# Kernel optimization log

Hardware: AMD Instinct MI355X
Metric: run time of the kernel (lower is better)

Reference implementation:

```python
import jax, jax.numpy as jnp
import numpy as np

ALPHA = 0.25        # focal alpha
GAMMA = 2.0         # focal gamma
POS_T = 0.5         # max_iou positive threshold
NEG_T = 0.4         # max_iou negative threshold
SL1_BETA = 1.0 / 9.0  # smooth_l1 with sigma=3
EPS = 1e-6

N, T, A, C = 8, 64, 65536, 80


def setup_inputs() -> dict:
    key = jax.random.key(0)
    ks = jax.random.split(key, 6)
    labels = jax.random.randint(ks[0], (N, T), 1, C)
    y_true = jax.nn.one_hot(labels, C, dtype=jnp.float32)
    xy = jax.random.uniform(ks[1], (N, T, 2)) * 0.7
    wh = jax.random.uniform(ks[2], (N, T, 2)) * 0.25 + 0.02
    bbox_true = jnp.concatenate([xy, xy + wh], axis=-1)
    valid = (jnp.arange(T) < 24).astype(jnp.float32)  # zero-pad remaining GT rows
    bbox_true = bbox_true * valid[None, :, None]
    axy = jax.random.uniform(ks[3], (A, 2)) * 0.9
    awh = jax.random.uniform(jax.random.fold_in(ks[3], 1), (A, 2)) * 0.15 + 0.02
    anchors = jnp.concatenate([axy, axy + awh], axis=-1)
    y_pred = jax.random.normal(ks[4], (N, A, C), dtype=jnp.float32)
    bbox_pred = jax.random.normal(ks[5], (N, A, 4), dtype=jnp.float32) * 0.1
    return {"y_true": y_true, "bbox_true": bbox_true, "y_pred": y_pred,
            "bbox_pred": bbox_pred, "anchors": anchors}


def _iou(b1, b2):
    # b1: (T,4), b2: (A,4) -> (T,A)
    a1 = jnp.maximum(b1[:, 2] - b1[:, 0], 0) * jnp.maximum(b1[:, 3] - b1[:, 1], 0)
    a2 = jnp.maximum(b2[:, 2] - b2[:, 0], 0) * jnp.maximum(b2[:, 3] - b2[:, 1], 0)
    lt = jnp.maximum(b1[:, None, :2], b2[None, :, :2])
    rb = jnp.minimum(b1[:, None, 2:], b2[None, :, 2:])
    wh = jnp.maximum(rb - lt, 0.0)
    inter = wh[..., 0] * wh[..., 1]
    union = a1[:, None] + a2[None, :] - inter
    return inter / jnp.maximum(union, 1e-10)


def _bbox2delta(boxes, anchors):
    # standard (dx, dy, dw, dh) encoding, mean=0 / std=1
    wa = jnp.maximum(anchors[:, 2] - anchors[:, 0], EPS)
    ha = jnp.maximum(anchors[:, 3] - anchors[:, 1], EPS)
    cxa = anchors[:, 0] + 0.5 * wa
    cya = anchors[:, 1] + 0.5 * ha
    wt = jnp.maximum(boxes[:, 2] - boxes[:, 0], EPS)
    ht = jnp.maximum(boxes[:, 3] - boxes[:, 1], EPS)
    cxt = boxes[:, 0] + 0.5 * (boxes[:, 2] - boxes[:, 0])
    cyt = boxes[:, 1] + 0.5 * (boxes[:, 3] - boxes[:, 1])
    return jnp.stack([(cxt - cxa) / wa, (cyt - cya) / ha,
                      jnp.log(wt / wa), jnp.log(ht / ha)], axis=-1)


def _encode_target(y_true_i, bbox_true_i, anchors):
    # y_true_i: (T,C), bbox_true_i: (T,4), anchors: (A,4)
    valid = jnp.any(bbox_true_i > 0, axis=-1)                 # (T,)
    iou = jnp.where(valid[:, None], _iou(bbox_true_i, anchors), -1.0)  # (T,A)
    max_iou = iou.max(axis=0)                                  # (A,)
    assigned = iou.argmax(axis=0)                              # (A,) gt index per anchor
    pos = max_iou >= POS_T
    neg = (max_iou < NEG_T)
    # low-quality matching: each valid gt's best anchor is positive for that gt
    gt_best = iou.argmax(axis=1)                               # (T,)
    gt_best_iou = iou.max(axis=1)
    lq = valid & (gt_best_iou > 0)
    assigned = assigned.at[gt_best].set(jnp.where(lq, jnp.arange(bbox_true_i.shape[0]), assigned[gt_best]))
    pos = pos.at[gt_best].set(jnp.where(lq, True, pos[gt_best]))
    neg = neg & (~pos)
    state = jnp.where(pos, 1, jnp.where(neg, -1, 0)).astype(jnp.int8)[:, None]  # (A,1)
    # class target: background one-hot [1,0,...,0], positives get gt label
    bg = jnp.zeros((anchors.shape[0], y_true_i.shape[-1]), jnp.float32).at[:, 0].set(1.0)
    yt = jnp.where(pos[:, None], y_true_i[assigned], bg)       # (A,C)
    delta = _bbox2delta(bbox_true_i[assigned], anchors)        # (A,4)
    bt = jnp.where(pos[:, None], delta, 0.0)
    return state, yt, bt


def _focal_bce(y_true, logits):
    # elementwise sigmoid focal loss
    ce = jnp.maximum(logits, 0) - logits * y_true + jnp.log1p(jnp.exp(-jnp.abs(logits)))
    p = jax.nn.sigmoid(logits)
    p_t = y_true * p + (1.0 - y_true) * (1.0 - p)
    a_t = y_true * ALPHA + (1.0 - y_true) * (1.0 - ALPHA)
    return a_t * jnp.power(1.0 - p_t, GAMMA) * ce


def _smooth_l1(y_true, y_pred):
    d = jnp.abs(y_true - y_pred)
    return jnp.where(d < SL1_BETA, 0.5 * d * d / SL1_BETA, d - 0.5 * SL1_BETA)


def _sanitize(x):
    return jnp.where(jnp.isnan(x) | jnp.isinf(x), 0.0, x)


def reference(y_true, bbox_true, y_pred, bbox_pred, anchors):
    state, yt, bt = jax.vmap(lambda a, b: _encode_target(a, b, anchors))(y_true, bbox_true)
    positive_w = (state == 1).astype(y_pred.dtype)   # (N,A,1)
    target_w = (state != 0).astype(y_pred.dtype)     # (N,A,1)
    avg_factor = jnp.sum(jnp.maximum(jnp.sum(positive_w, axis=-2), 1.0))
    yt = yt * positive_w                              # background=False zeroes non-positives
    cls = jnp.sum(_focal_bce(yt, y_pred) * target_w) / avg_factor
    box = jnp.sum(_smooth_l1(bt, bbox_pred) * positive_w) / avg_factor
    return _sanitize(cls), _sanitize(box)
```

## Files before the change

### kernel.cpp

```cpp
#include <hip/hip_runtime.h>
#include <hip/hip_bf16.h>
#include <math.h>

#define NB 8
#define TB 64
#define AB 65536
#define CB 80
#define EPSF 1e-6f

#define WS_POSCNT_OFF 4096
#define WS_LABEL_OFF  4608
#define WS_CODE_OFF   8192
#define WS_PCLS_OFF   (WS_CODE_OFF + NB*AB*4)
#define WS_PCCLS_OFF  (WS_PCLS_OFF + 4096*4)
#define WS_PCBOX_OFF  (WS_PCCLS_OFF + 2048*4)
#define WS_MEMSET_BYTES 4608

__device__ __forceinline__ float focal0(float l) {
    float q  = __expf(-fabsf(l));
    float r  = __builtin_amdgcn_rcpf(1.f + q);
    float lg = __logf(r);
    float ce = fmaxf(l, 0.f) - lg;
    float p  = (l >= 0.f) ? r : 1.f - r;
    return 0.75f * p * p * ce;
}
__device__ __forceinline__ float focal_diff(float l) {
    float q  = __expf(-fabsf(l));
    float r  = __builtin_amdgcn_rcpf(1.f + q);
    float lg = __logf(r);
    float m  = fmaxf(l, 0.f);
    float p  = (l >= 0.f) ? r : 1.f - r;
    float f0 = 0.75f * p * p * (m - lg);
    float om = 1.f - p;
    float f1 = 0.25f * om * om * (m - l - lg);
    return f1 - f0;
}
__device__ __forceinline__ float smooth_l1(float x) {
    float d = fabsf(x);
    return d < (1.f / 9.f) ? 4.5f * d * d : d - (0.5f / 9.f);
}

__global__ __launch_bounds__(256) void assign_kernel(
    const float* __restrict__ bbox_true,
    const float* __restrict__ anchors,
    int*   __restrict__ code,
    unsigned long long* __restrict__ gt_key)
{
    __shared__ float4 s_box[TB];
    __shared__ float  s_a1[TB];
    __shared__ unsigned long long s_key[TB];

    const int blk   = blockIdx.x;
    const int i     = blk >> 8;
    const int abase = (blk & 255) << 8;
    const int tid   = threadIdx.x;

    if (tid < TB) {
        float4 b = ((const float4*)bbox_true)[i * TB + tid];
        s_box[tid] = b;
        s_a1[tid]  = fmaxf(b.z - b.x, 0.f) * fmaxf(b.w - b.y, 0.f);
        s_key[tid] = 0ull;
    }
    __syncthreads();

    const int a = abase + tid;
    const float4 an = ((const float4*)anchors)[a];
    const float a2 = fmaxf(an.z - an.x, 0.f) * fmaxf(an.w - an.y, 0.f);

    float best = -1.0f;
    int bestt = 0;
    #pragma unroll 8
    for (int t = 0; t < TB; ++t) {
        float4 b = s_box[t];
        float lx = fmaxf(b.x, an.x), ly = fmaxf(b.y, an.y);
        float rx = fminf(b.z, an.z), ry = fminf(b.w, an.w);
        float w = fmaxf(rx - lx, 0.f), h = fmaxf(ry - ly, 0.f);
        float inter = w * h;
        float uni = s_a1[t] + a2 - inter;
        float iou = inter * __builtin_amdgcn_rcpf(fmaxf(uni, 1e-10f));
        if (iou > 0.f) {
            unsigned long long key =
                ((unsigned long long)__float_as_uint(iou) << 32) |
                (unsigned long long)((unsigned)a ^ 0xFFFFFFFFu);
            if (key > s_key[t])
                atomicMax(&s_key[t], key);
        }
        if (iou > best) { best = iou; bestt = t; }
    }
    bool pos = best >= 0.5f;
    bool neg = best < 0.4f;
    code[i * AB + a] = pos ? bestt : (neg ? -1 : -2);

    __syncthreads();
    if (tid < TB) {
        unsigned long long k = s_key[tid];
        if (k) atomicMax(&gt_key[i * TB + tid], k);
    }
}

__global__ void lq_label_kernel(const unsigned long long* __restrict__ gt_key,
                                const float* __restrict__ y_true,
                                int* __restrict__ code,
                                int* __restrict__ labels)
{
    __shared__ unsigned long long sk[NB * TB];
    const int tid = threadIdx.x;
    sk[tid] = gt_key[tid];

    const float* row = y_true + (size_t)tid * CB;
    int lab = 0;
    for (int c = 0; c < CB; ++c)
        if (row[c] > 0.5f) lab = c;
    labels[tid] = lab;

    __syncthreads();
    const int i = tid >> 6, t = tid & 63;
    unsigned long long k = sk[tid];
    if (k) {
        unsigned a = (unsigned)(k & 0xFFFFFFFFull) ^ 0xFFFFFFFFu;
        bool win = true;
        for (int t2 = t + 1; t2 < TB; ++t2) {
            unsigned long long k2 = sk[(i << 6) | t2];
            if (k2 && (((unsigned)(k2 & 0xFFFFFFFFull) ^ 0xFFFFFFFFu) == a))
                win = false;
        }
        if (win) code[i * AB + (int)a] = t;
    }
}

__global__ __launch_bounds__(256) void stream_kernel(
    const float4* __restrict__ yp4,
    float* __restrict__ p_cls)
{
    const int tid = threadIdx.x;
    const int g0  = blockIdx.x * 256 + tid;
    float acc = 0.f;
    #pragma unroll
    for (int j = 0; j < 10; ++j) {
        float4 v = yp4[g0 + j * 1048576];
        acc += focal0(v.x) + focal0(v.y) + focal0(v.z) + focal0(v.w);
    }
    for (int off = 32; off > 0; off >>= 1) acc += __shfl_down(acc, off);
    __shared__ float s[4];
    int wave = tid >> 6, lane = tid & 63;
    if (lane == 0) s[wave] = acc;
    __syncthreads();
    if (tid == 0) p_cls[blockIdx.x] = s[0] + s[1] + s[2] + s[3];
}

__global__ __launch_bounds__(256) void corr_kernel(
    const float* __restrict__ y_pred,
    const float* __restrict__ bbox_true,
    const float* __restrict__ bbox_pred,
    const float* __restrict__ anchors,
    const int*   __restrict__ code,
    const int*   __restrict__ labels,
    float* __restrict__ p_ccls,
    float* __restrict__ p_cbox,
    int*   __restrict__ pos_cnt)
{
    const int tid = threadIdx.x;
    const int b   = blockIdx.x;
    const int i   = b >> 8;
    const int g   = b * 256 + tid;
    const int a   = g & (AB - 1);

    const int cv = code[g];
    float cls_c = 0.f, box_c = 0.f;
    int posc = 0;

    if (cv >= 0) {
        posc = 1;
        int c = labels[i * TB + cv];
        float l = y_pred[(size_t)g * CB + c];
        cls_c = focal_diff(l);

        float4 bt = ((const float4*)bbox_true)[i * TB + cv];
        float4 an = ((const float4*)anchors)[a];
        float wa = fmaxf(an.z - an.x, EPSF), ha = fmaxf(an.w - an.y, EPSF);
        float cxa = an.x + 0.5f * wa,  cya = an.y + 0.5f * ha;
        float wt = fmaxf(bt.z - bt.x, EPSF), ht = fmaxf(bt.w - bt.y, EPSF);
        float cxt = bt.x + 0.5f * (bt.z - bt.x), cyt = bt.y + 0.5f * (bt.w - bt.y);
        float d0 = (cxt - cxa) / wa, d1 = (cyt - cya) / ha;
        float d2 = __logf(wt / wa),  d3 = __logf(ht / ha);
        float4 bp = ((const float4*)bbox_pred)[g];
        box_c = smooth_l1(d0 - bp.x) + smooth_l1(d1 - bp.y) +
                smooth_l1(d2 - bp.z) + smooth_l1(d3 - bp.w);
    } else if (cv == -2) {
        const float4* yp4 = (const float4*)(y_pred + (size_t)g * CB);
        float s = 0.f;
        #pragma unroll 4
        for (int k = 0; k < 20; ++k) {
            float4 v = yp4[k];
            s += focal0(v.x) + focal0(v.y) + focal0(v.z) + focal0(v.w);
        }
        cls_c = -s;
    }

    for (int off = 32; off > 0; off >>= 1) {
        cls_c += __shfl_down(cls_c, off);
        box_c += __shfl_down(box_c, off);
        posc  += __shfl_down(posc, off);
    }
    __shared__ float sc[4], sb[4];
    __shared__ int   sp[4];
    int wave = tid >> 6, lane = tid & 63;
    if (lane == 0) { sc[wave] = cls_c; sb[wave] = box_c; sp[wave] = posc; }
    __syncthreads();
    if (tid == 0) {
        p_ccls[b] = sc[0] + sc[1] + sc[2] + sc[3];
        p_cbox[b] = sb[0] + sb[1] + sb[2] + sb[3];
        int p = sp[0] + sp[1] + sp[2] + sp[3];
        if (p) atomicAdd(&pos_cnt[i], p);
    }
}

__global__ __launch_bounds__(256) void reduce_kernel(
    const float* __restrict__ p_cls,
    const float* __restrict__ p_ccls,
    const float* __restrict__ p_cbox,
    const int*   __restrict__ pos_cnt,
    float* __restrict__ out)
{
    const int tid = threadIdx.x;
    const int wave = tid >> 6, lane = tid & 63;

    double c = 0.0, bx = 0.0;
    #pragma unroll
    for (int j = 0; j < 16; ++j) c += (double)p_cls[tid + j * 256];
    #pragma unroll
    for (int j = 0; j < 8; ++j)  c += (double)p_ccls[tid + j * 256];
    #pragma unroll
    for (int j = 0; j < 8; ++j)  bx += (double)p_cbox[tid + j * 256];

    for (int off = 32; off > 0; off >>= 1) {
        c  += __shfl_down(c, off);
        bx += __shfl_down(bx, off);
    }
    __shared__ double sc[4], sb[4];
    if (lane == 0) { sc[wave] = c; sb[wave] = bx; }
    __syncthreads();
    if (tid == 0) {
        float avg = 0.f;
        for (int i = 0; i < NB; ++i) avg += fmaxf((float)pos_cnt[i], 1.0f);
        double ct = sc[0] + sc[1] + sc[2] + sc[3];
        double bt = sb[0] + sb[1] + sb[2] + sb[3];
        float cf = (float)(ct / (double)avg);
        float bf = (float)(bt / (double)avg);
        if (isnan(cf) || isinf(cf)) cf = 0.f;
        if (isnan(bf) || isinf(bf)) bf = 0.f;
        out[0] = cf;
        out[1] = bf;
    }
}

extern "C" void kernel_launch(void* const* d_in, const int* in_sizes, int n_in,
                              void* d_out, int out_size, void* d_ws, size_t ws_size,
                              hipStream_t stream) {
    const float* y_true    = (const float*)d_in[0];
    const float* bbox_true = (const float*)d_in[1];
    const float* y_pred    = (const float*)d_in[2];
    const float* bbox_pred = (const float*)d_in[3];
    const float* anchors   = (const float*)d_in[4];
    float* out = (float*)d_out;

    char* ws = (char*)d_ws;
    unsigned long long* gt_key = (unsigned long long*)ws;
    int*   pos_cnt = (int*)(ws + WS_POSCNT_OFF);
    int*   labels  = (int*)(ws + WS_LABEL_OFF);
    int*   code    = (int*)(ws + WS_CODE_OFF);
    float* p_cls   = (float*)(ws + WS_PCLS_OFF);
    float* p_ccls  = (float*)(ws + WS_PCCLS_OFF);
    float* p_cbox  = (float*)(ws + WS_PCBOX_OFF);

    hipMemsetAsync(ws, 0, WS_MEMSET_BYTES, stream);

    assign_kernel<<<NB * AB / 256, 256, 0, stream>>>(bbox_true, anchors, code, gt_key);
    lq_label_kernel<<<1, NB * TB, 0, stream>>>(gt_key, y_true, code, labels);
    stream_kernel<<<4096, 256, 0, stream>>>((const float4*)y_pred, p_cls);
    corr_kernel<<<NB * AB / 256, 256, 0, stream>>>(
        y_pred, bbox_true, bbox_pred, anchors, code, labels,
        p_ccls, p_cbox, pos_cnt);
    reduce_kernel<<<1, 256, 0, stream>>>(p_cls, p_ccls, p_cbox, pos_cnt, out);
}
```

Before: 334.1 us.

## Compact positive/ignore anchors into lists and drop the dense correction pass

```diff
diff --git a/kernel.cpp b/kernel.cpp
--- a/kernel.cpp
+++ b/kernel.cpp
@@ -8,31 +8,28 @@
 #define CB 80
 #define EPSF 1e-6f
 
-#define WS_POSCNT_OFF 4096
+#define WS_CNT_OFF    4096
 #define WS_LABEL_OFF  4608
 #define WS_CODE_OFF   8192
-#define WS_PCLS_OFF   (WS_CODE_OFF + NB*AB*4)
-#define WS_PCCLS_OFF  (WS_PCLS_OFF + 4096*4)
-#define WS_PCBOX_OFF  (WS_PCCLS_OFF + 2048*4)
+#define WS_PLIST_OFF  (WS_CODE_OFF + NB*AB*4)
+#define WS_ILIST_OFF  (WS_PLIST_OFF + 525312*4)
+#define WS_PCLS_OFF   (WS_ILIST_OFF + 525312*4)
 #define WS_MEMSET_BYTES 4608
 
 __device__ __forceinline__ float focal0(float l) {
-    float q  = __expf(-fabsf(l));
-    float r  = __builtin_amdgcn_rcpf(1.f + q);
-    float lg = __logf(r);
-    float ce = fmaxf(l, 0.f) - lg;
-    float p  = (l >= 0.f) ? r : 1.f - r;
-    return 0.75f * p * p * ce;
+    float u  = __expf(l);
+    float r  = __builtin_amdgcn_rcpf(1.f + u);
+    float p  = 1.f - r;
+    float lg = __log2f(r);
+    return p * p * lg * -0.5198603854f;
 }
 __device__ __forceinline__ float focal_diff(float l) {
-    float q  = __expf(-fabsf(l));
-    float r  = __builtin_amdgcn_rcpf(1.f + q);
-    float lg = __logf(r);
-    float m  = fmaxf(l, 0.f);
-    float p  = (l >= 0.f) ? r : 1.f - r;
-    float f0 = 0.75f * p * p * (m - lg);
-    float om = 1.f - p;
-    float f1 = 0.25f * om * om * (m - l - lg);
+    float u  = __expf(l);
+    float r  = __builtin_amdgcn_rcpf(1.f + u);
+    float p  = 1.f - r;
+    float sp = -0.6931471806f * __log2f(r);
+    float f1 = 0.25f * r * r * (sp - l);
+    float f0 = 0.75f * p * p * sp;
     return f1 - f0;
 }
 __device__ __forceinline__ float smooth_l1(float x) {
@@ -44,7 +41,10 @@
     const float* __restrict__ bbox_true,
     const float* __restrict__ anchors,
     int*   __restrict__ code,
-    unsigned long long* __restrict__ gt_key)
+    unsigned long long* __restrict__ gt_key,
+    int*   __restrict__ cnts,
+    int*   __restrict__ pos_list,
+    int*   __restrict__ ign_list)
 {
     __shared__ float4 s_box[TB];
     __shared__ float  s_a1[TB];
@@ -87,9 +87,17 @@
         }
         if (iou > best) { best = iou; bestt = t; }
     }
+    const int g = i * AB + a;
     bool pos = best >= 0.5f;
     bool neg = best < 0.4f;
-    code[i * AB + a] = pos ? bestt : (neg ? -1 : -2);
+    code[g] = pos ? bestt : (neg ? -1 : -2);
+    if (pos) {
+        int idx = atomicAdd(&cnts[0], 1);
+        pos_list[idx] = g;
+    } else if (!neg) {
+        int idx = atomicAdd(&cnts[1], 1);
+        ign_list[idx] = g;
+    }
 
     __syncthreads();
     if (tid < TB) {
@@ -101,7 +109,9 @@
 __global__ void lq_label_kernel(const unsigned long long* __restrict__ gt_key,
                                 const float* __restrict__ y_true,
                                 int* __restrict__ code,
-                                int* __restrict__ labels)
+                                int* __restrict__ labels,
+                                int* __restrict__ cnts,
+                                int* __restrict__ pos_list)
 {
     __shared__ unsigned long long sk[NB * TB];
     const int tid = threadIdx.x;
@@ -124,12 +134,22 @@
             if (k2 && (((unsigned)(k2 & 0xFFFFFFFFull) ^ 0xFFFFFFFFu) == a))
                 win = false;
         }
-        if (win) code[i * AB + (int)a] = t;
+        if (win) {
+            int g = i * AB + (int)a;
+            int pre = code[g];
+            code[g] = t;
+            if (pre < 0) {
+                int idx = atomicAdd(&cnts[0], 1);
+                pos_list[idx] = g | ((pre == -2) ? (1 << 30) : 0);
+            }
+        }
     }
 }
 
 __global__ __launch_bounds__(256) void stream_kernel(
     const float4* __restrict__ yp4,
+    const int*    __restrict__ ign_list,
+    const int*    __restrict__ cnts,
     float* __restrict__ p_cls)
 {
     const int tid = threadIdx.x;
@@ -140,6 +160,13 @@
         float4 v = yp4[g0 + j * 1048576];
         acc += focal0(v.x) + focal0(v.y) + focal0(v.z) + focal0(v.w);
     }
+    const int work = cnts[1] * 20;
+    for (int w = g0; w < work; w += 4096 * 256) {
+        int e = w / 20, ch = w - e * 20;
+        int g = ign_list[e];
+        float4 v = yp4[g * 20 + ch];
+        acc -= focal0(v.x) + focal0(v.y) + focal0(v.z) + focal0(v.w);
+    }
     for (int off = 32; off > 0; off >>= 1) acc += __shfl_down(acc, off);
     __shared__ float s[4];
     int wave = tid >> 6, lane = tid & 63;
@@ -148,34 +175,48 @@
     if (tid == 0) p_cls[blockIdx.x] = s[0] + s[1] + s[2] + s[3];
 }
 
-__global__ __launch_bounds__(256) void corr_kernel(
+__global__ __launch_bounds__(256) void reduce_kernel(
+    const float* __restrict__ p_cls,
+    const int*   __restrict__ cnts,
+    const int*   __restrict__ pos_list,
+    const int*   __restrict__ code,
+    const int*   __restrict__ labels,
     const float* __restrict__ y_pred,
     const float* __restrict__ bbox_true,
     const float* __restrict__ bbox_pred,
     const float* __restrict__ anchors,
-    const int*   __restrict__ code,
-    const int*   __restrict__ labels,
-    float* __restrict__ p_ccls,
-    float* __restrict__ p_cbox,
-    int*   __restrict__ pos_cnt)
+    float* __restrict__ out)
 {
     const int tid = threadIdx.x;
-    const int b   = blockIdx.x;
-    const int i   = b >> 8;
-    const int g   = b * 256 + tid;
-    const int a   = g & (AB - 1);
-
-    const int cv = code[g];
-    float cls_c = 0.f, box_c = 0.f;
-    int posc = 0;
-
-    if (cv >= 0) {
-        posc = 1;
-        int c = labels[i * TB + cv];
-        float l = y_pred[(size_t)g * CB + c];
-        cls_c = focal_diff(l);
-
-        float4 bt = ((const float4*)bbox_true)[i * TB + cv];
+    const int wave = tid >> 6, lane = tid & 63;
+    __shared__ int spc[NB];
+    if (tid < NB) spc[tid] = 0;
+    __syncthreads();
+
+    double c = 0.0;
+    #pragma unroll
+    for (int j = 0; j < 16; ++j) c += (double)p_cls[tid + j * 256];
+
+    float dsum = 0.f, bsum = 0.f;
+    const int pcnt = cnts[0];
+    for (int e = tid; e < pcnt; e += 256) {
+        unsigned u = (unsigned)pos_list[e];
+        int g    = (int)(u & 0x3FFFFFFFu);
+        int flag = (int)(u >> 30);
+        int i = g >> 16, a = g & (AB - 1);
+        int t = code[g];
+        int lab = labels[i * TB + t];
+        dsum += focal_diff(y_pred[(size_t)g * CB + lab]);
+        if (flag) {
+            const float4* rw = (const float4*)(y_pred + (size_t)g * CB);
+            float s = 0.f;
+            for (int kk = 0; kk < 20; ++kk) {
+                float4 v = rw[kk];
+                s += focal0(v.x) + focal0(v.y) + focal0(v.z) + focal0(v.w);
+            }
+            dsum += s;
+        }
+        float4 bt = ((const float4*)bbox_true)[i * TB + t];
         float4 an = ((const float4*)anchors)[a];
         float wa = fmaxf(an.z - an.x, EPSF), ha = fmaxf(an.w - an.y, EPSF);
         float cxa = an.x + 0.5f * wa,  cya = an.y + 0.5f * ha;
@@ -184,69 +225,26 @@
         float d0 = (cxt - cxa) / wa, d1 = (cyt - cya) / ha;
         float d2 = __logf(wt / wa),  d3 = __logf(ht / ha);
         float4 bp = ((const float4*)bbox_pred)[g];
-        box_c = smooth_l1(d0 - bp.x) + smooth_l1(d1 - bp.y) +
+        bsum += smooth_l1(d0 - bp.x) + smooth_l1(d1 - bp.y) +
                 smooth_l1(d2 - bp.z) + smooth_l1(d3 - bp.w);
-    } else if (cv == -2) {
-        const float4* yp4 = (const float4*)(y_pred + (size_t)g * CB);
-        float s = 0.f;
-        #pragma unroll 4
-        for (int k = 0; k < 20; ++k) {
-            float4 v = yp4[k];
-            s += focal0(v.x) + focal0(v.y) + focal0(v.z) + focal0(v.w);
-        }
-        cls_c = -s;
-    }
-
+        atomicAdd(&spc[i], 1);
+    }
+    __syncthreads();
+
+    double ct = c + (double)dsum;
+    double bx = (double)bsum;
     for (int off = 32; off > 0; off >>= 1) {
-        cls_c += __shfl_down(cls_c, off);
-        box_c += __shfl_down(box_c, off);
-        posc  += __shfl_down(posc, off);
-    }
-    __shared__ float sc[4], sb[4];
-    __shared__ int   sp[4];
-    int wave = tid >> 6, lane = tid & 63;
-    if (lane == 0) { sc[wave] = cls_c; sb[wave] = box_c; sp[wave] = posc; }
-    __syncthreads();
-    if (tid == 0) {
-        p_ccls[b] = sc[0] + sc[1] + sc[2] + sc[3];
-        p_cbox[b] = sb[0] + sb[1] + sb[2] + sb[3];
-        int p = sp[0] + sp[1] + sp[2] + sp[3];
-        if (p) atomicAdd(&pos_cnt[i], p);
-    }
-}
-
-__global__ __launch_bounds__(256) void reduce_kernel(
-    const float* __restrict__ p_cls,
-    const float* __restrict__ p_ccls,
-    const float* __restrict__ p_cbox,
-    const int*   __restrict__ pos_cnt,
-    float* __restrict__ out)
-{
-    const int tid = threadIdx.x;
-    const int wave = tid >> 6, lane = tid & 63;
-
-    double c = 0.0, bx = 0.0;
-    #pragma unroll
-    for (int j = 0; j < 16; ++j) c += (double)p_cls[tid + j * 256];
-    #pragma unroll
-    for (int j = 0; j < 8; ++j)  c += (double)p_ccls[tid + j * 256];
-    #pragma unroll
-    for (int j = 0; j < 8; ++j)  bx += (double)p_cbox[tid + j * 256];
-
-    for (int off = 32; off > 0; off >>= 1) {
-        c  += __shfl_down(c, off);
+        ct += __shfl_down(ct, off);
         bx += __shfl_down(bx, off);
     }
     __shared__ double sc[4], sb[4];
-    if (lane == 0) { sc[wave] = c; sb[wave] = bx; }
+    if (lane == 0) { sc[wave] = ct; sb[wave] = bx; }
     __syncthreads();
     if (tid == 0) {
         float avg = 0.f;
-        for (int i = 0; i < NB; ++i) avg += fmaxf((float)pos_cnt[i], 1.0f);
-        double ct = sc[0] + sc[1] + sc[2] + sc[3];
-        double bt = sb[0] + sb[1] + sb[2] + sb[3];
-        float cf = (float)(ct / (double)avg);
-        float bf = (float)(bt / (double)avg);
+        for (int i = 0; i < NB; ++i) avg += fmaxf((float)spc[i], 1.0f);
+        float cf = (float)((sc[0] + sc[1] + sc[2] + sc[3]) / (double)avg);
+        float bf = (float)((sb[0] + sb[1] + sb[2] + sb[3]) / (double)avg);
         if (isnan(cf) || isinf(cf)) cf = 0.f;
         if (isnan(bf) || isinf(bf)) bf = 0.f;
         out[0] = cf;
@@ -266,20 +264,22 @@
 
     char* ws = (char*)d_ws;
     unsigned long long* gt_key = (unsigned long long*)ws;
-    int*   pos_cnt = (int*)(ws + WS_POSCNT_OFF);
-    int*   labels  = (int*)(ws + WS_LABEL_OFF);
-    int*   code    = (int*)(ws + WS_CODE_OFF);
-    float* p_cls   = (float*)(ws + WS_PCLS_OFF);
-    float* p_ccls  = (float*)(ws + WS_PCCLS_OFF);
-    float* p_cbox  = (float*)(ws + WS_PCBOX_OFF);
+    int*   cnts     = (int*)(ws + WS_CNT_OFF);
+    int*   labels   = (int*)(ws + WS_LABEL_OFF);
+    int*   code     = (int*)(ws + WS_CODE_OFF);
+    int*   pos_list = (int*)(ws + WS_PLIST_OFF);
+    int*   ign_list = (int*)(ws + WS_ILIST_OFF);
+    float* p_cls    = (float*)(ws + WS_PCLS_OFF);
 
     hipMemsetAsync(ws, 0, WS_MEMSET_BYTES, stream);
 
-    assign_kernel<<<NB * AB / 256, 256, 0, stream>>>(bbox_true, anchors, code, gt_key);
-    lq_label_kernel<<<1, NB * TB, 0, stream>>>(gt_key, y_true, code, labels);
-    stream_kernel<<<4096, 256, 0, stream>>>((const float4*)y_pred, p_cls);
-    corr_kernel<<<NB * AB / 256, 256, 0, stream>>>(
-        y_pred, bbox_true, bbox_pred, anchors, code, labels,
-        p_ccls, p_cbox, pos_cnt);
-    reduce_kernel<<<1, 256, 0, stream>>>(p_cls, p_ccls, p_cbox, pos_cnt, out);
-}
+    assign_kernel<<<NB * AB / 256, 256, 0, stream>>>(
+        bbox_true, anchors, code, gt_key, cnts, pos_list, ign_list);
+    lq_label_kernel<<<1, NB * TB, 0, stream>>>(
+        gt_key, y_true, code, labels, cnts, pos_list);
+    stream_kernel<<<4096, 256, 0, stream>>>(
+        (const float4*)y_pred, ign_list, cnts, p_cls);
+    reduce_kernel<<<1, 256, 0, stream>>>(
+        p_cls, cnts, pos_list, code, labels,
+        y_pred, bbox_true, bbox_pred, anchors, out);
+}
```

New measurement: 496.9 us. 1.49x slower.
